# Kernel optimization log

Measured on AMD Instinct MI355X. Metric: run time of the kernel, lower is better.

Reference implementation:

```python
import jax, jax.numpy as jnp
import numpy as np

B, S, D = 2, 2048, 1024
H = 16
HD = D // H  # 64
ROPE_BASE = 10000.0


def rotate_half(x):
    x1, x2 = jnp.split(x, 2, axis=-1)
    return jnp.concatenate((-x2, x1), axis=-1)


def rope_cos_sin(seq_len, dim, dtype):
    inv_freq = 1.0 / (ROPE_BASE ** (jnp.arange(0, dim, 2, dtype=jnp.float32) / dim))
    t = jnp.arange(seq_len, dtype=jnp.float32)
    freqs = jnp.einsum('i,j->ij', t, inv_freq)          # [S, dim/2]
    emb = jnp.concatenate((freqs, freqs), axis=-1)      # [S, dim]
    return jnp.cos(emb).astype(dtype), jnp.sin(emb).astype(dtype)


def setup_inputs() -> dict:
    key = jax.random.key(0)
    ks = jax.random.split(key, 5)
    std = 0.02
    return {
        'x': jax.random.normal(ks[0], (B, S, D), dtype=jnp.float32),
        'wq': jax.random.normal(ks[1], (D, D), dtype=jnp.float32) * std,
        'wk': jax.random.normal(ks[2], (D, D), dtype=jnp.float32) * std,
        'wv': jax.random.normal(ks[3], (D, D), dtype=jnp.float32) * std,
        'wo': jax.random.normal(ks[4], (D, D), dtype=jnp.float32) * std,
    }


def reference(x, wq, wk, wv, wo):
    b, s, d = x.shape
    # Q/K/V projections (nn.Linear: x @ W.T)
    q = jnp.einsum('bsd,ed->bse', x, wq).reshape(b, s, H, HD).transpose(0, 2, 1, 3)
    k = jnp.einsum('bsd,ed->bse', x, wk).reshape(b, s, H, HD).transpose(0, 2, 1, 3)
    v = jnp.einsum('bsd,ed->bse', x, wv).reshape(b, s, H, HD).transpose(0, 2, 1, 3)
    # RoPE
    cos, sin = rope_cos_sin(s, HD, x.dtype)  # [s, HD]
    cos = cos[None, None]  # [1,1,s,HD]
    sin = sin[None, None]
    q = q * cos + rotate_half(q) * sin
    k = k * cos + rotate_half(k) * sin
    # Causal SDPA
    scale = HD ** -0.5
    scores = jnp.einsum('bhqd,bhkd->bhqk', q, k) * scale
    causal = jnp.tril(jnp.ones((s, s), dtype=bool))
    scores = jnp.where(causal[None, None], scores, jnp.finfo(scores.dtype).min)
    attn = jax.nn.softmax(scores, axis=-1)
    out = jnp.einsum('bhqk,bhkd->bhqd', attn, v)
    out = out.transpose(0, 2, 1, 3).reshape(b, s, d)
    return jnp.einsum('bsd,ed->bse', out, wo)
```

## Files before the change

### kernel.cpp

```cpp
#include <hip/hip_runtime.h>
#include <hip/hip_bf16.h>
#include <cstdint>
#include <cstddef>

#define BDIM 2
#define SDIM 2048
#define DDIM 1024
#define HN   16
#define HDIM 64

using bf16 = __bf16;
typedef __attribute__((ext_vector_type(8))) __bf16 bf16x8;
typedef __attribute__((ext_vector_type(4))) __bf16 bf16x4;
typedef __attribute__((ext_vector_type(8))) unsigned short ushort8;
typedef __attribute__((ext_vector_type(4))) float  f32x4;

#define MFMA16(a, b, c) __builtin_amdgcn_mfma_f32_16x16x32_bf16((a), (b), (c), 0, 0, 0)

#define ASYNC16(g, l)                                                          \
  __builtin_amdgcn_global_load_lds(                                            \
      (const __attribute__((address_space(1))) void*)(g),                      \
      (__attribute__((address_space(3))) void*)(l), 16, 0, 0)

#define QSCALE 0.1803368801111204f

__global__ __launch_bounds__(256) void cvt_bf16(const float* __restrict__ src,
                                                bf16* __restrict__ dst, int n4) {
  int i = blockIdx.x * 256 + threadIdx.x;
  if (i < n4) {
    float4 v = ((const float4*)src)[i];
    bf16x4 o = {(__bf16)v.x, (__bf16)v.y, (__bf16)v.z, (__bf16)v.w};
    *(bf16x4*)(dst + (size_t)i * 4) = o;
  }
}

struct Ptr4 { const float* p[4]; };
__global__ __launch_bounds__(256) void cvt_w(Ptr4 srcs, bf16* __restrict__ dst) {
  const int seg = blockIdx.y;
  const float* src = srcs.p[seg];
  int i = blockIdx.x * 256 + threadIdx.x;
  float4 v = ((const float4*)src)[i];
  bf16x4 o = {(__bf16)v.x, (__bf16)v.y, (__bf16)v.z, (__bf16)v.w};
  *(bf16x4*)(dst + (size_t)seg * (DDIM * DDIM) + (size_t)i * 4) = o;
}

__global__ __launch_bounds__(256) void rope_table(float* __restrict__ cosT,
                                                  float* __restrict__ sinT) {
  int i = blockIdx.x * 256 + threadIdx.x;
  int s = i >> 5, j = i & 31;
  float inv = powf(10000.f, -(float)j * (1.f / 32.f));
  float a = (float)s * inv;
  float sn, c;
  sincosf(a, &sn, &c);
  cosT[s * 64 + j]      = c;
  cosT[s * 64 + j + 32] = c;
  sinT[s * 64 + j]      = sn;
  sinT[s * 64 + j + 32] = sn;
}

__global__ __launch_bounds__(256) void fixup_qkv(bf16* __restrict__ q,
                                                 bf16* __restrict__ k,
                                                 const unsigned short* __restrict__ v,
                                                 unsigned short* __restrict__ vt,
                                                 const float* __restrict__ cosT,
                                                 const float* __restrict__ sinT) {
  const int bh = blockIdx.y;
  const int s0 = blockIdx.x * 32;
  const int tid = threadIdx.x;

  {
    const int s = s0 + (tid >> 3);
    const int j0 = (tid & 7) * 4;
    const size_t base = ((size_t)bh * SDIM + s) * HDIM;
    const float4 c4 = *(const float4*)(cosT + s * 64 + j0);
    const float4 s4 = *(const float4*)(sinT + s * 64 + j0);
    const float cc[4] = {c4.x, c4.y, c4.z, c4.w};
    const float ss[4] = {s4.x, s4.y, s4.z, s4.w};

    bf16x4 qlo = *(bf16x4*)(q + base + j0);
    bf16x4 qhi = *(bf16x4*)(q + base + j0 + 32);
    bf16x4 klo = *(bf16x4*)(k + base + j0);
    bf16x4 khi = *(bf16x4*)(k + base + j0 + 32);
    bf16x4 rql, rqh, rkl, rkh;
#pragma unroll
    for (int e = 0; e < 4; ++e) {
      float a = (float)qlo[e], b = (float)qhi[e];
      rql[e] = (__bf16)((a * cc[e] - b * ss[e]) * QSCALE);
      rqh[e] = (__bf16)((b * cc[e] + a * ss[e]) * QSCALE);
      a = (float)klo[e]; b = (float)khi[e];
      rkl[e] = (__bf16)(a * cc[e] - b * ss[e]);
      rkh[e] = (__bf16)(b * cc[e] + a * ss[e]);
    }
    *(bf16x4*)(q + base + j0)      = rql;
    *(bf16x4*)(q + base + j0 + 32) = rqh;
    *(bf16x4*)(k + base + j0)      = rkl;
    *(bf16x4*)(k + base + j0 + 32) = rkh;
  }

  {
    const int w = tid >> 6, d = tid & 63;
    const int sb = s0 + w * 8;
    const unsigned short* src = v + ((size_t)bh * SDIM + sb) * HDIM + d;
    ushort8 o;
#pragma unroll
    for (int j = 0; j < 8; ++j) o[j] = src[(size_t)j * HDIM];
    *(ushort8*)(vt + ((size_t)bh * HDIM + d) * SDIM + sb) = o;
  }
}

template <int MODE>
__global__ __launch_bounds__(256) void gemm_bt(const bf16* __restrict__ A,
                                               const bf16* __restrict__ B0,
                                               void* __restrict__ C0) {
  constexpr int K = 1024;
  __shared__ __align__(16) bf16 As[128 * 64];
  __shared__ __align__(16) bf16 Bs[128 * 64];
  const int tid = threadIdx.x;
  const int l = tid & 63, w = tid >> 6;
  const int wr = w >> 1, wc = w & 1;
  const int lr = l & 15, lg = l >> 4;
  const int bm = blockIdx.y * 128;
  const int bn = blockIdx.x * 128;
  const bf16* Bw = B0 + (size_t)blockIdx.z * (1024 * 1024);

  f32x4 acc[4][4] = {};

  for (int k0 = 0; k0 < K; k0 += 64) {
    __syncthreads();
#pragma unroll
    for (int i = 0; i < 4; ++i) {
      int idx = i * 2048 + tid * 8;
      int row = idx >> 6, col = idx & 63;
      ASYNC16(A + (size_t)(bm + row) * K + (k0 + col), As + idx);
      ASYNC16(Bw + (size_t)(bn + row) * K + (k0 + col), Bs + idx);
    }
    __syncthreads();
#pragma unroll
    for (int c = 0; c < 2; ++c) {
      bf16x8 af[4], bfr[4];
#pragma unroll
      for (int m = 0; m < 4; ++m)
        af[m] = *(const bf16x8*)(As + (wr * 64 + m * 16 + lr) * 64 + c * 32 + lg * 8);
#pragma unroll
      for (int n = 0; n < 4; ++n)
        bfr[n] = *(const bf16x8*)(Bs + (wc * 64 + n * 16 + lr) * 64 + c * 32 + lg * 8);
      __builtin_amdgcn_s_setprio(1);
#pragma unroll
      for (int m = 0; m < 4; ++m)
#pragma unroll
        for (int n = 0; n < 4; ++n)
          acc[m][n] = MFMA16(af[m], bfr[n], acc[m][n]);
      __builtin_amdgcn_s_setprio(0);
    }
  }

#pragma unroll
  for (int m = 0; m < 4; ++m) {
#pragma unroll
    for (int n = 0; n < 4; ++n) {
#pragma unroll
      for (int r = 0; r < 4; ++r) {
        int row = bm + wr * 64 + m * 16 + lg * 4 + r;
        int col = bn + wc * 64 + n * 16 + lr;
        float v = acc[m][n][r];
        if constexpr (MODE == 0) {
          bf16* C = (bf16*)C0 + (size_t)blockIdx.z * ((size_t)BDIM * SDIM * DDIM);
          size_t off = (((size_t)(row >> 11) * HN + (col >> 6)) * SDIM + (row & (SDIM - 1))) * HDIM + (col & 63);
          C[off] = (__bf16)v;
        } else {
          ((float*)C0)[(size_t)row * DDIM + col] = v;
        }
      }
    }
  }
}

__global__ __launch_bounds__(256) void attn_fwd(const bf16* __restrict__ qg,
                                                const bf16* __restrict__ kg,
                                                const bf16* __restrict__ vtg,
                                                bf16* __restrict__ og) {
  __shared__ __align__(16) bf16 Sl[3][4096];
  __shared__ __align__(16) bf16 Pl[4][1024];

  const int tid = threadIdx.x;
  const int l = tid & 63, w = tid >> 6;
  const int lr = l & 15, lg = l >> 4;
  const int bh = blockIdx.x;
  const int qt = 31 - blockIdx.y;
  const int q0 = qt * 64;
  const size_t hb = (size_t)bh * SDIM * HDIM;
  const bf16* Q  = qg + hb;
  const bf16* Kp = kg + hb;
  const bf16* Vp = vtg + hb;
  const int b = bh >> 4, h = bh & 15;
  bf16* Pw = &Pl[w][0];
  const int swz = lr & 7;

  const int mm0 = 2 * w, mm1 = 2 * w + 1;
  const int f0 = mm0 & 3, c0 = mm0 >> 2;
  const int f1 = mm1 & 3, c1 = mm1 >> 2;
  const int lo0 = mm0 * 512 + l * 8;
  const int lo1 = mm1 * 512 + l * 8;

  bf16x8 qf[2];
#pragma unroll
  for (int c = 0; c < 2; ++c)
    qf[c] = *(const bf16x8*)(Q + (size_t)(q0 + w * 16 + lr) * HDIM + c * 32 + lg * 8);

  f32x4 o[4] = {};
  float m = -3e38f, lsum = 0.f;

  const bf16* kN0 = Kp + (size_t)(f0 * 16 + lr) * HDIM + c0 * 32 + lg * 8;
  const bf16* kN1 = Kp + (size_t)(f1 * 16 + lr) * HDIM + c1 * 32 + lg * 8;
  const bf16* vN0 = Vp + (size_t)(f0 * 16 + lr) * SDIM + c0 * 32 + lg * 8;
  const bf16* vN1 = Vp + (size_t)(f1 * 16 + lr) * SDIM + c1 * 32 + lg * 8;

  ASYNC16(kN0, Sl[0] + lo0); kN0 += 64 * HDIM;
  ASYNC16(kN1, Sl[0] + lo1); kN1 += 64 * HDIM;
  ASYNC16(vN0, Sl[1] + lo0); vN0 += 64;
  ASYNC16(vN1, Sl[1] + lo1); vN1 += 64;
  __syncthreads();

  int ks = 0, vs = 1;
  for (int t = 0; t <= qt; ++t) {
    const int kn = 3 - ks - vs;
    if (t < qt) {
      ASYNC16(kN0, Sl[kn] + lo0); kN0 += 64 * HDIM;
      ASYNC16(kN1, Sl[kn] + lo1); kN1 += 64 * HDIM;
    }

    const bool diag = (t == qt);
    const int fLim = diag ? w : 3;

    f32x4 sc[4] = {};
    __builtin_amdgcn_s_setprio(1);
#pragma unroll
    for (int c = 0; c < 2; ++c)
#pragma unroll
      for (int f = 0; f < 4; ++f)
        if (f <= fLim) {
          bf16x8 kfr = *(const bf16x8*)(Sl[ks] + (c * 4 + f) * 512 + l * 8);
          sc[f] = MFMA16(kfr, qf[c], sc[f]);
        }
    __builtin_amdgcn_s_setprio(0);

    __syncthreads();
    if (t < qt) {
      ASYNC16(vN0, Sl[ks] + lo0); vN0 += 64;
      ASYNC16(vN1, Sl[ks] + lo1); vN1 += 64;
    }

    if (diag) {
#pragma unroll
      for (int f = 0; f < 4; ++f)
#pragma unroll
        for (int r = 0; r < 4; ++r) {
          if (f > w)
            sc[f][r] = -3e38f;
          else if (f == w)
            sc[f][r] = (lg * 4 + r <= lr) ? sc[f][r] : -3e38f;
        }
    }

    float mxl = -3e38f;
#pragma unroll
    for (int f = 0; f < 4; ++f)
#pragma unroll
      for (int r = 0; r < 4; ++r) mxl = fmaxf(mxl, sc[f][r]);

    if (!__all(mxl - m <= 8.f)) {
      float mx = fmaxf(mxl, __shfl_xor(mxl, 16));
      mx = fmaxf(mx, __shfl_xor(mx, 32));
      float mnew = fmaxf(m, mx);
      float corr = exp2f(m - mnew);
      m = mnew;
      lsum *= corr;
      float cb[4];
#pragma unroll
      for (int r = 0; r < 4; ++r) cb[r] = __shfl(corr, lg * 4 + r);
#pragma unroll
      for (int n = 0; n < 4; ++n)
#pragma unroll
        for (int r = 0; r < 4; ++r) o[n][r] *= cb[r];
    }

    float rs = 0.f;
#pragma unroll
    for (int f = 0; f < 4; ++f) {
      float p0 = exp2f(sc[f][0] - m);
      float p1 = exp2f(sc[f][1] - m);
      float p2 = exp2f(sc[f][2] - m);
      float p3 = exp2f(sc[f][3] - m);
      rs += (p0 + p1) + (p2 + p3);
      bf16x4 pv = {(__bf16)p0, (__bf16)p1, (__bf16)p2, (__bf16)p3};
      const int ch = f * 2 + (lg >> 1);
      *(bf16x4*)(Pw + lr * 64 + ((ch ^ swz) << 3) + (lg & 1) * 4) = pv;
    }
    rs += __shfl_xor(rs, 16);
    rs += __shfl_xor(rs, 32);
    lsum += rs;

    const int cLim = diag ? (w >> 1) : 1;
    __builtin_amdgcn_s_setprio(1);
#pragma unroll
    for (int c = 0; c < 2; ++c)
      if (c <= cLim) {
        bf16x8 pf = *(const bf16x8*)(Pw + lr * 64 + (((c * 4 + lg) ^ swz) << 3));
#pragma unroll
        for (int n = 0; n < 4; ++n) {
          bf16x8 vfr = *(const bf16x8*)(Sl[vs] + (c * 4 + n) * 512 + l * 8);
          o[n] = MFMA16(pf, vfr, o[n]);
        }
      }
    __builtin_amdgcn_s_setprio(0);

    __syncthreads();
    vs = ks;
    ks = kn;
  }

  float lb[4];
#pragma unroll
  for (int r = 0; r < 4; ++r) lb[r] = __shfl(lsum, lg * 4 + r);
#pragma unroll
  for (int r = 0; r < 4; ++r) {
    float rl = 1.f / lb[r];
    int qr = q0 + 16 * w + lg * 4 + r;
#pragma unroll
    for (int n = 0; n < 4; ++n)
      og[((size_t)(b * SDIM + qr)) * DDIM + h * HDIM + n * 16 + lr] =
          (__bf16)(o[n][r] * rl);
  }
}

extern "C" void kernel_launch(void* const* d_in, const int* in_sizes, int n_in,
                              void* d_out, int out_size, void* d_ws, size_t ws_size,
                              hipStream_t stream) {
  const float* x  = (const float*)d_in[0];
  const float* wq = (const float*)d_in[1];
  const float* wk = (const float*)d_in[2];
  const float* wv = (const float*)d_in[3];
  const float* wo = (const float*)d_in[4];

  char* ws = (char*)d_ws;
  const size_t MB = 1024 * 1024;
  bf16* xb   = (bf16*)(ws + 0);
  bf16* wqb  = (bf16*)(ws + 8 * MB);
  bf16* wob  = (bf16*)(ws + 14 * MB);
  bf16* qb   = (bf16*)(ws + 16 * MB);
  bf16* kb   = (bf16*)(ws + 24 * MB);
  bf16* vb   = (bf16*)(ws + 32 * MB);
  bf16* ob   = (bf16*)(ws + 40 * MB);
  float* cosT = (float*)(ws + 48 * MB);
  float* sinT = (float*)(ws + 49 * MB);
  bf16* vtb  = xb;

  const int NX = BDIM * SDIM * DDIM;
  const int NW = DDIM * DDIM;

  cvt_bf16<<<NX / 4 / 256, 256, 0, stream>>>(x, xb, NX / 4);
  Ptr4 wsrc{{wq, wk, wv, wo}};
  cvt_w<<<dim3(NW / 4 / 256, 4), 256, 0, stream>>>(wsrc, wqb);
  rope_table<<<(SDIM * 32) / 256, 256, 0, stream>>>(cosT, sinT);
  gemm_bt<0><<<dim3(8, 32, 3), 256, 0, stream>>>(xb, wqb, (void*)qb);
  fixup_qkv<<<dim3(SDIM / 32, 32), 256, 0, stream>>>(qb, kb, (const unsigned short*)vb,
                                                     (unsigned short*)vtb, cosT, sinT);
  attn_fwd<<<dim3(32, 32), 256, 0, stream>>>(qb, kb, vtb, ob);
  gemm_bt<1><<<dim3(8, 32, 1), 256, 0, stream>>>(ob, wob, d_out);
}
```

Before: 142.5 us.

## Split attention KV loop across two wave groups with in-block softmax merge

After: 137.7 us. 1.03x faster.

```diff
diff --git a/kernel.cpp b/kernel.cpp
--- a/kernel.cpp
+++ b/kernel.cpp
@@ -175,15 +175,16 @@
   }
 }
 
-__global__ __launch_bounds__(256) void attn_fwd(const bf16* __restrict__ qg,
+__global__ __launch_bounds__(512) void attn_fwd(const bf16* __restrict__ qg,
                                                 const bf16* __restrict__ kg,
                                                 const bf16* __restrict__ vtg,
                                                 bf16* __restrict__ og) {
-  __shared__ __align__(16) bf16 Sl[3][4096];
-  __shared__ __align__(16) bf16 Pl[4][1024];
+  __shared__ __align__(16) bf16 Sl[2][3][4096];
+  __shared__ __align__(16) bf16 Pl[8][1024];
 
   const int tid = threadIdx.x;
   const int l = tid & 63, w = tid >> 6;
+  const int g = w >> 2, wg = w & 3;
   const int lr = l & 15, lg = l >> 4;
   const int bh = blockIdx.x;
   const int qt = 31 - blockIdx.y;
@@ -196,140 +197,181 @@
   bf16* Pw = &Pl[w][0];
   const int swz = lr & 7;
 
-  const int mm0 = 2 * w, mm1 = 2 * w + 1;
+  const int mm0 = 2 * wg, mm1 = 2 * wg + 1;
   const int f0 = mm0 & 3, c0 = mm0 >> 2;
   const int f1 = mm1 & 3, c1 = mm1 >> 2;
   const int lo0 = mm0 * 512 + l * 8;
   const int lo1 = mm1 * 512 + l * 8;
+  bf16* const SlG = &Sl[g][0][0];
 
   bf16x8 qf[2];
 #pragma unroll
   for (int c = 0; c < 2; ++c)
-    qf[c] = *(const bf16x8*)(Q + (size_t)(q0 + w * 16 + lr) * HDIM + c * 32 + lg * 8);
+    qf[c] = *(const bf16x8*)(Q + (size_t)(q0 + wg * 16 + lr) * HDIM + c * 32 + lg * 8);
 
   f32x4 o[4] = {};
   float m = -3e38f, lsum = 0.f;
 
-  const bf16* kN0 = Kp + (size_t)(f0 * 16 + lr) * HDIM + c0 * 32 + lg * 8;
-  const bf16* kN1 = Kp + (size_t)(f1 * 16 + lr) * HDIM + c1 * 32 + lg * 8;
-  const bf16* vN0 = Vp + (size_t)(f0 * 16 + lr) * SDIM + c0 * 32 + lg * 8;
-  const bf16* vN1 = Vp + (size_t)(f1 * 16 + lr) * SDIM + c1 * 32 + lg * 8;
-
-  ASYNC16(kN0, Sl[0] + lo0); kN0 += 64 * HDIM;
-  ASYNC16(kN1, Sl[0] + lo1); kN1 += 64 * HDIM;
-  ASYNC16(vN0, Sl[1] + lo0); vN0 += 64;
-  ASYNC16(vN1, Sl[1] + lo1); vN1 += 64;
+  const int ng   = (qt >= g) ? ((qt - g) >> 1) + 1 : 0;
+  const int smax = (qt >> 1) + 1;
+
+  const bf16* kN0 = Kp + (size_t)(f0 * 16 + lr) * HDIM + c0 * 32 + lg * 8 + (size_t)g * 64 * HDIM;
+  const bf16* kN1 = Kp + (size_t)(f1 * 16 + lr) * HDIM + c1 * 32 + lg * 8 + (size_t)g * 64 * HDIM;
+  const bf16* vN0 = Vp + (size_t)(f0 * 16 + lr) * SDIM + c0 * 32 + lg * 8 + g * 64;
+  const bf16* vN1 = Vp + (size_t)(f1 * 16 + lr) * SDIM + c1 * 32 + lg * 8 + g * 64;
+
+  if (ng > 0) {
+    ASYNC16(kN0, SlG + 0 * 4096 + lo0); kN0 += 128 * HDIM;
+    ASYNC16(kN1, SlG + 0 * 4096 + lo1); kN1 += 128 * HDIM;
+    ASYNC16(vN0, SlG + 1 * 4096 + lo0); vN0 += 128;
+    ASYNC16(vN1, SlG + 1 * 4096 + lo1); vN1 += 128;
+  }
   __syncthreads();
 
   int ks = 0, vs = 1;
-  for (int t = 0; t <= qt; ++t) {
+  for (int s = 0; s < smax; ++s) {
+    const int t = 2 * s + g;
+    const bool act = (s < ng);
     const int kn = 3 - ks - vs;
-    if (t < qt) {
-      ASYNC16(kN0, Sl[kn] + lo0); kN0 += 64 * HDIM;
-      ASYNC16(kN1, Sl[kn] + lo1); kN1 += 64 * HDIM;
+    const bool hasNext = act && (s + 1 < ng);
+
+    if (hasNext) {
+      ASYNC16(kN0, SlG + kn * 4096 + lo0); kN0 += 128 * HDIM;
+      ASYNC16(kN1, SlG + kn * 4096 + lo1); kN1 += 128 * HDIM;
     }
 
     const bool diag = (t == qt);
-    const int fLim = diag ? w : 3;
+    const int fLim = diag ? wg : 3;
 
     f32x4 sc[4] = {};
-    __builtin_amdgcn_s_setprio(1);
-#pragma unroll
-    for (int c = 0; c < 2; ++c)
+    if (act) {
+      __builtin_amdgcn_s_setprio(1);
+#pragma unroll
+      for (int c = 0; c < 2; ++c)
+#pragma unroll
+        for (int f = 0; f < 4; ++f)
+          if (f <= fLim) {
+            bf16x8 kfr = *(const bf16x8*)(SlG + ks * 4096 + (c * 4 + f) * 512 + l * 8);
+            sc[f] = MFMA16(kfr, qf[c], sc[f]);
+          }
+      __builtin_amdgcn_s_setprio(0);
+    }
+
+    __syncthreads();
+    if (hasNext) {
+      ASYNC16(vN0, SlG + ks * 4096 + lo0); vN0 += 128;
+      ASYNC16(vN1, SlG + ks * 4096 + lo1); vN1 += 128;
+    }
+
+    if (act) {
+      if (diag) {
+#pragma unroll
+        for (int f = 0; f < 4; ++f)
+#pragma unroll
+          for (int r = 0; r < 4; ++r) {
+            if (f > wg)
+              sc[f][r] = -3e38f;
+            else if (f == wg)
+              sc[f][r] = (lg * 4 + r <= lr) ? sc[f][r] : -3e38f;
+          }
+      }
+
+      float mxl = -3e38f;
 #pragma unroll
       for (int f = 0; f < 4; ++f)
-        if (f <= fLim) {
-          bf16x8 kfr = *(const bf16x8*)(Sl[ks] + (c * 4 + f) * 512 + l * 8);
-          sc[f] = MFMA16(kfr, qf[c], sc[f]);
+#pragma unroll
+        for (int r = 0; r < 4; ++r) mxl = fmaxf(mxl, sc[f][r]);
+
+      if (!__all(mxl - m <= 8.f)) {
+        float mx = fmaxf(mxl, __shfl_xor(mxl, 16));
+        mx = fmaxf(mx, __shfl_xor(mx, 32));
+        float mnew = fmaxf(m, mx);
+        float corr = exp2f(m - mnew);
+        m = mnew;
+        lsum *= corr;
+        float cb[4];
+#pragma unroll
+        for (int r = 0; r < 4; ++r) cb[r] = __shfl(corr, lg * 4 + r);
+#pragma unroll
+        for (int n = 0; n < 4; ++n)
+#pragma unroll
+          for (int r = 0; r < 4; ++r) o[n][r] *= cb[r];
+      }
+
+      float rs = 0.f;
+#pragma unroll
+      for (int f = 0; f < 4; ++f) {
+        float p0 = exp2f(sc[f][0] - m);
+        float p1 = exp2f(sc[f][1] - m);
+        float p2 = exp2f(sc[f][2] - m);
+        float p3 = exp2f(sc[f][3] - m);
+        rs += (p0 + p1) + (p2 + p3);
+        bf16x4 pv = {(__bf16)p0, (__bf16)p1, (__bf16)p2, (__bf16)p3};
+        const int ch = f * 2 + (lg >> 1);
+        *(bf16x4*)(Pw + lr * 64 + ((ch ^ swz) << 3) + (lg & 1) * 4) = pv;
+      }
+      rs += __shfl_xor(rs, 16);
+      rs += __shfl_xor(rs, 32);
+      lsum += rs;
+
+      const int cLim = diag ? (wg >> 1) : 1;
+      __builtin_amdgcn_s_setprio(1);
+#pragma unroll
+      for (int c = 0; c < 2; ++c)
+        if (c <= cLim) {
+          bf16x8 pf = *(const bf16x8*)(Pw + lr * 64 + (((c * 4 + lg) ^ swz) << 3));
+#pragma unroll
+          for (int n = 0; n < 4; ++n) {
+            bf16x8 vfr = *(const bf16x8*)(SlG + vs * 4096 + (c * 4 + n) * 512 + l * 8);
+            o[n] = MFMA16(pf, vfr, o[n]);
+          }
         }
-    __builtin_amdgcn_s_setprio(0);
-
-    __syncthreads();
-    if (t < qt) {
-      ASYNC16(vN0, Sl[ks] + lo0); vN0 += 64;
-      ASYNC16(vN1, Sl[ks] + lo1); vN1 += 64;
-    }
-
-    if (diag) {
-#pragma unroll
-      for (int f = 0; f < 4; ++f)
-#pragma unroll
-        for (int r = 0; r < 4; ++r) {
-          if (f > w)
-            sc[f][r] = -3e38f;
-          else if (f == w)
-            sc[f][r] = (lg * 4 + r <= lr) ? sc[f][r] : -3e38f;
-        }
-    }
-
-    float mxl = -3e38f;
-#pragma unroll
-    for (int f = 0; f < 4; ++f)
-#pragma unroll
-      for (int r = 0; r < 4; ++r) mxl = fmaxf(mxl, sc[f][r]);
-
-    if (!__all(mxl - m <= 8.f)) {
-      float mx = fmaxf(mxl, __shfl_xor(mxl, 16));
-      mx = fmaxf(mx, __shfl_xor(mx, 32));
-      float mnew = fmaxf(m, mx);
-      float corr = exp2f(m - mnew);
-      m = mnew;
-      lsum *= corr;
-      float cb[4];
-#pragma unroll
-      for (int r = 0; r < 4; ++r) cb[r] = __shfl(corr, lg * 4 + r);
-#pragma unroll
-      for (int n = 0; n < 4; ++n)
-#pragma unroll
-        for (int r = 0; r < 4; ++r) o[n][r] *= cb[r];
-    }
-
-    float rs = 0.f;
-#pragma unroll
-    for (int f = 0; f < 4; ++f) {
-      float p0 = exp2f(sc[f][0] - m);
-      float p1 = exp2f(sc[f][1] - m);
-      float p2 = exp2f(sc[f][2] - m);
-      float p3 = exp2f(sc[f][3] - m);
-      rs += (p0 + p1) + (p2 + p3);
-      bf16x4 pv = {(__bf16)p0, (__bf16)p1, (__bf16)p2, (__bf16)p3};
-      const int ch = f * 2 + (lg >> 1);
-      *(bf16x4*)(Pw + lr * 64 + ((ch ^ swz) << 3) + (lg & 1) * 4) = pv;
-    }
-    rs += __shfl_xor(rs, 16);
-    rs += __shfl_xor(rs, 32);
-    lsum += rs;
-
-    const int cLim = diag ? (w >> 1) : 1;
-    __builtin_amdgcn_s_setprio(1);
-#pragma unroll
-    for (int c = 0; c < 2; ++c)
-      if (c <= cLim) {
-        bf16x8 pf = *(const bf16x8*)(Pw + lr * 64 + (((c * 4 + lg) ^ swz) << 3));
-#pragma unroll
-        for (int n = 0; n < 4; ++n) {
-          bf16x8 vfr = *(const bf16x8*)(Sl[vs] + (c * 4 + n) * 512 + l * 8);
-          o[n] = MFMA16(pf, vfr, o[n]);
-        }
-      }
-    __builtin_amdgcn_s_setprio(0);
+      __builtin_amdgcn_s_setprio(0);
+    }
 
     __syncthreads();
     vs = ks;
     ks = kn;
   }
 
-  float lb[4];
-#pragma unroll
-  for (int r = 0; r < 4; ++r) lb[r] = __shfl(lsum, lg * 4 + r);
-#pragma unroll
-  for (int r = 0; r < 4; ++r) {
-    float rl = 1.f / lb[r];
-    int qr = q0 + 16 * w + lg * 4 + r;
+  float* Osh = (float*)&Sl[0][0][0];
+  float* Msh = Osh + 4096;
+  float* Lsh = Msh + 256;
+
+  if (g == 1) {
+    Msh[wg * 64 + l] = m;
+    Lsh[wg * 64 + l] = lsum;
 #pragma unroll
     for (int n = 0; n < 4; ++n)
-      og[((size_t)(b * SDIM + qr)) * DDIM + h * HDIM + n * 16 + lr] =
-          (__bf16)(o[n][r] * rl);
+#pragma unroll
+      for (int r = 0; r < 4; ++r)
+        Osh[((wg * 4 + n) * 4 + r) * 64 + l] = o[n][r];
+  }
+  __syncthreads();
+
+  if (g == 0) {
+    float m1 = Msh[wg * 64 + l], l1 = Lsh[wg * 64 + l];
+    float mt = fmaxf(m, m1);
+    float a0 = exp2f(m - mt), a1 = exp2f(m1 - mt);
+    float lt = lsum * a0 + l1 * a1;
+    float a0b[4], a1b[4], ltb[4];
+#pragma unroll
+    for (int r = 0; r < 4; ++r) {
+      a0b[r] = __shfl(a0, lg * 4 + r);
+      a1b[r] = __shfl(a1, lg * 4 + r);
+      ltb[r] = __shfl(lt, lg * 4 + r);
+    }
+#pragma unroll
+    for (int r = 0; r < 4; ++r) {
+      float rl = 1.f / ltb[r];
+      int qr = q0 + 16 * wg + lg * 4 + r;
+#pragma unroll
+      for (int n = 0; n < 4; ++n) {
+        float o1 = Osh[((wg * 4 + n) * 4 + r) * 64 + l];
+        og[((size_t)(b * SDIM + qr)) * DDIM + h * HDIM + n * 16 + lr] =
+            (__bf16)((o[n][r] * a0b[r] + o1 * a1b[r]) * rl);
+      }
+    }
   }
 }
 
@@ -365,6 +407,6 @@
   gemm_bt<0><<<dim3(8, 32, 3), 256, 0, stream>>>(xb, wqb, (void*)qb);
   fixup_qkv<<<dim3(SDIM / 32, 32), 256, 0, stream>>>(qb, kb, (const unsigned short*)vb,
                                                      (unsigned short*)vtb, cosT, sinT);
-  attn_fwd<<<dim3(32, 32), 256, 0, stream>>>(qb, kb, vtb, ob);
+  attn_fwd<<<dim3(32, 32), 512, 0, stream>>>(qb, kb, vtb, ob);
   gemm_bt<1><<<dim3(8, 32, 1), 256, 0, stream>>>(ob, wob, d_out);
 }
```
